# Kernel tuning notes

Hardware: AMD Instinct MI355X
Metric: run time of the kernel (lower is better)

## Reference

```python
import jax, jax.numpy as jnp
import numpy as np


def setup_inputs() -> dict:
    key = jax.random.key(0)
    k1, k2 = jax.random.split(key)
    T, D, K = 100000, 768, 500  # frames, feature dim (HuBERT base), k-means clusters
    feat = jax.random.normal(k1, (T, D), dtype=jnp.float32)
    C = jax.random.normal(k2, (D, K), dtype=jnp.float32)  # cluster centers, transposed as in module
    return {"feat": feat, "C": C}


def reference(feat, C):
    # Squared euclidean distance expanded: ||f||^2 - 2 f.C + ||c||^2
    Cnorm = jnp.sum(C * C, axis=0, keepdims=True)            # [1, K]
    fnorm = jnp.sum(feat * feat, axis=1, keepdims=True)       # [T, 1]
    dist = fnorm - 2.0 * jnp.matmul(feat, C) + Cnorm          # [T, K]
    return jnp.argmin(dist, axis=1)[None, :]                  # [1, T] cluster ids
```

## Files before the change

### kernel.cpp

```cpp
#include <hip/hip_runtime.h>
#include <float.h>

#define D_DIM 768
#define K_DIM 500
#define NDT   24
#define BM    64
#define NTH   256
#define PB_STRIDE 100352

typedef _Float16 f16x8  __attribute__((ext_vector_type(8)));
typedef float    f32x16 __attribute__((ext_vector_type(16)));


__global__ void cnorm_partial_kernel(const float* __restrict__ C,
                                     double* __restrict__ partial, int K) {
    const int k = threadIdx.x;
    const int w = blockIdx.x;
    double s = 0.0;
    if (k < K) {
        const int d0 = w * (D_DIM / 16);
        for (int d = d0; d < d0 + (D_DIM / 16); ++d) {
            const float c = C[(size_t)d * K + k];
            s = fma((double)c, (double)c, s);
        }
    }
    partial[w * 512 + k] = s;
}

__global__ void cnorm_finish_kernel(const double* __restrict__ partial,
                                    float* __restrict__ cnorm, int K) {
    const int k = threadIdx.x;
    if (k < K) {
        double s = 0.0;
        for (int w = 0; w < 16; ++w) s += partial[w * 512 + k];
        cnorm[k] = (float)s;
    } else {
        cnorm[k] = FLT_MAX;
    }
}

__global__ void packB_kernel(const float* __restrict__ C,
                             _Float16* __restrict__ BpH,
                             _Float16* __restrict__ BpL) {
    const int idx = blockIdx.x * 256 + threadIdx.x;
    const int col = idx & 511;
    const int dt  = idx >> 9;
    f16x8 h[4], l[4];
    #pragma unroll
    for (int c = 0; c < 4; ++c)
        #pragma unroll
        for (int j = 0; j < 8; ++j) {
            const int k = c * 8 + j;
            const float v = (col < K_DIM)
                          ? C[(size_t)(dt * 32 + k) * K_DIM + col] : 0.0f;
            const _Float16 hh = (_Float16)v;
            h[c][j] = hh;
            l[c][j] = (_Float16)(v - (float)hh);
        }
    f16x8* dH = (f16x8*)(BpH + ((size_t)dt * 512 + col) * 32);
    f16x8* dL = (f16x8*)(BpL + ((size_t)dt * 512 + col) * 32);
    #pragma unroll
    for (int c = 0; c < 4; ++c) { dH[c] = h[c]; dL[c] = l[c]; }
}

__launch_bounds__(NTH, 3)
__global__ void assign_kernel(const float* __restrict__ feat,
                              const _Float16* __restrict__ BpH,
                              const _Float16* __restrict__ BpL,
                              const float* __restrict__ cnorm,
                              float* __restrict__ pbv,
                              int* __restrict__ pbi,
                              int T) {
    __shared__ __align__(16) _Float16 AsH[2][BM * 32];
    __shared__ __align__(16) _Float16 AsL[2][BM * 32];
    __shared__ float red_v[BM * 4];
    __shared__ int   red_i[BM * 4];

    const int tid  = threadIdx.x;
    const int wn   = tid >> 6;
    const int lane = tid & 63;
    const int c5   = lane & 31;
    const int kh   = lane >> 5;
    const int bid  = blockIdx.x;
    const int half = bid & 1;
    const int R0   = (bid >> 1) * BM;

    const int ar = tid >> 2;
    const int ac = (tid & 3) << 3;
    const bool arow_ok = (R0 + ar) < T;
    const float* fptr = feat + (size_t)(R0 + ar) * D_DIM + ac;
    const int asl = ((ac >> 3) + (ar >> 1)) & 3;

    const int colbase = half * 256 + wn * 64 + c5;
    const _Float16* bpH = BpH + (size_t)colbase * 32 + kh * 8;
    const _Float16* bpL = BpL + (size_t)colbase * 32 + kh * 8;

    f32x16 acc[2][2];
    #pragma unroll
    for (int m = 0; m < 2; ++m)
        #pragma unroll
        for (int n = 0; n < 2; ++n)
            #pragma unroll
            for (int r = 0; r < 16; ++r) acc[m][n][r] = 0.0f;

    {
        float4 v0 = make_float4(0.f, 0.f, 0.f, 0.f), v1 = v0;
        if (arow_ok) {
            v0 = *(const float4*)(fptr);
            v1 = *(const float4*)(fptr + 4);
        }
        const float fa[8] = {v0.x, v0.y, v0.z, v0.w, v1.x, v1.y, v1.z, v1.w};
        f16x8 h, l;
        #pragma unroll
        for (int j = 0; j < 8; ++j) {
            const _Float16 hh = (_Float16)fa[j];
            h[j] = hh; l[j] = (_Float16)(fa[j] - (float)hh);
        }
        ((f16x8*)AsH[0])[ar * 4 + asl] = h;
        ((f16x8*)AsL[0])[ar * 4 + asl] = l;
    }
    __syncthreads();

    for (int dt = 0; dt < NDT; ++dt) {
        const int cur = dt & 1;
        const bool hasNext = (dt + 1) < NDT;

        const size_t bo = (size_t)dt * 16384;
        f16x8 bH[2][2], bL[2][2];
        #pragma unroll
        for (int n = 0; n < 2; ++n)
            #pragma unroll
            for (int step = 0; step < 2; ++step) {
                bH[n][step] = *(const f16x8*)(bpH + bo + n * 1024 + step * 16);
                bL[n][step] = *(const f16x8*)(bpL + bo + n * 1024 + step * 16);
            }

        float4 v0 = make_float4(0.f, 0.f, 0.f, 0.f), v1 = v0;
        if (hasNext && arow_ok) {
            v0 = *(const float4*)(fptr + (dt + 1) * 32);
            v1 = *(const float4*)(fptr + (dt + 1) * 32 + 4);
        }

        f16x8 aH[2][2], aL[2][2];
        #pragma unroll
        for (int m = 0; m < 2; ++m) {
            const int row = m * 32 + c5;
            #pragma unroll
            for (int step = 0; step < 2; ++step) {
                const int chunk = step * 2 + kh;
                const int sl = (chunk + (row >> 1)) & 3;
                aH[m][step] = ((const f16x8*)AsH[cur])[row * 4 + sl];
                aL[m][step] = ((const f16x8*)AsL[cur])[row * 4 + sl];
            }
        }

        __builtin_amdgcn_s_setprio(1);
        #pragma unroll
        for (int step = 0; step < 2; ++step)
            #pragma unroll
            for (int n = 0; n < 2; ++n)
                #pragma unroll
                for (int m = 0; m < 2; ++m) {
                    f32x16 a = acc[m][n];
                    a = __builtin_amdgcn_mfma_f32_32x32x16_f16(aH[m][step], bH[n][step], a, 0, 0, 0);
                    a = __builtin_amdgcn_mfma_f32_32x32x16_f16(aL[m][step], bH[n][step], a, 0, 0, 0);
                    a = __builtin_amdgcn_mfma_f32_32x32x16_f16(aH[m][step], bL[n][step], a, 0, 0, 0);
                    acc[m][n] = a;
                }
        __builtin_amdgcn_s_setprio(0);

        if (hasNext) {
            const float fa[8] = {v0.x, v0.y, v0.z, v0.w, v1.x, v1.y, v1.z, v1.w};
            f16x8 h, l;
            #pragma unroll
            for (int j = 0; j < 8; ++j) {
                const _Float16 hh = (_Float16)fa[j];
                h[j] = hh; l[j] = (_Float16)(fa[j] - (float)hh);
            }
            ((f16x8*)AsH[cur ^ 1])[ar * 4 + asl] = h;
            ((f16x8*)AsL[cur ^ 1])[ar * 4 + asl] = l;
        }
        __syncthreads();
    }

    float cn[2];
    #pragma unroll
    for (int n = 0; n < 2; ++n)
        cn[n] = cnorm[half * 256 + wn * 64 + n * 32 + c5];

    #pragma unroll
    for (int m = 0; m < 2; ++m) {
        #pragma unroll
        for (int r = 0; r < 16; ++r) {
            float best = cn[0] - 2.0f * acc[m][0][r];
            int   bi   = colbase;
            {
                const float s = cn[1] - 2.0f * acc[m][1][r];
                const int col = colbase + 32;
                if (s < best) { best = s; bi = col; }
            }
            #pragma unroll
            for (int msk = 1; msk < 32; msk <<= 1) {
                const float ov = __shfl_xor(best, msk, 64);
                const int   oi = __shfl_xor(bi,   msk, 64);
                if (ov < best || (ov == best && oi < bi)) { best = ov; bi = oi; }
            }
            if (c5 == 0) {
                const int rl = m * 32 + 4 * kh + (r & 3) + 8 * (r >> 2);
                red_v[rl * 4 + wn] = best;
                red_i[rl * 4 + wn] = bi;
            }
        }
    }
    __syncthreads();

    if (tid < BM) {
        float bv = red_v[tid * 4];
        int   bi = red_i[tid * 4];
        #pragma unroll
        for (int w = 1; w < 4; ++w) {
            const float v = red_v[tid * 4 + w];
            const int   i = red_i[tid * 4 + w];
            if (v < bv || (v == bv && i < bi)) { bv = v; bi = i; }
        }
        const int r = R0 + tid;
        if (r < T) {
            pbv[(size_t)half * PB_STRIDE + r] = bv;
            pbi[(size_t)half * PB_STRIDE + r] = bi;
        }
    }
}

__global__ void combine_kernel(const float* __restrict__ pbv,
                               const int* __restrict__ pbi,
                               int* __restrict__ out, int T) {
    const int r = blockIdx.x * 256 + threadIdx.x;
    if (r < T) {
        const float s0 = pbv[r];
        const int   i0 = pbi[r];
        const float s1 = pbv[PB_STRIDE + r];
        const int   i1 = pbi[PB_STRIDE + r];
        out[r] = (s1 < s0) ? i1 : i0;
    }
}

extern "C" void kernel_launch(void* const* d_in, const int* in_sizes, int n_in,
                              void* d_out, int out_size, void* d_ws, size_t ws_size,
                              hipStream_t stream) {
    const float* feat = (const float*)d_in[0];
    const float* C    = (const float*)d_in[1];
    int* out          = (int*)d_out;
    const int T = in_sizes[0] / D_DIM;
    const int K = in_sizes[1] / D_DIM;

    float*     cnorm   = (float*)d_ws;
    double*    partial = (double*)((char*)d_ws + 4096);
    _Float16*  BpH     = (_Float16*)((char*)d_ws + 131072);
    _Float16*  BpL     = (_Float16*)((char*)d_ws + 917504);
    float*     pbv     = (float*)((char*)d_ws + 1703936);
    int*       pbi     = (int*)((char*)d_ws + 2506752);

    hipLaunchKernelGGL(cnorm_partial_kernel, dim3(16), dim3(512), 0, stream,
                       C, partial, K);
    hipLaunchKernelGGL(cnorm_finish_kernel, dim3(1), dim3(512), 0, stream,
                       partial, cnorm, K);
    hipLaunchKernelGGL(packB_kernel, dim3(48), dim3(256), 0, stream,
                       C, BpH, BpL);

    const int nrb = (T + BM - 1) / BM;
    hipLaunchKernelGGL(assign_kernel, dim3(nrb * 2), dim3(NTH), 0, stream,
                       feat, BpH, BpL, cnorm, pbv, pbi, T);
    hipLaunchKernelGGL(combine_kernel, dim3((T + 255) / 256), dim3(256), 0, stream,
                       pbv, pbi, out, T);
}
```

Baseline: 326.3 us.

## Load feature operand directly from global into registers, dropping LDS staging

The A operand is no longer staged through double-buffered shared memory with a per-step barrier. Each lane now reads its own rows of feat straight from global memory and splits them into fp16 hi/lo parts in registers. This removes the LDS traffic and the __syncthreads per K step. In exchange, each of the four waves redundantly loads and converts the same 64 rows, so global/L2 reads of feat rise about fourfold, and loads are no longer prefetched one step ahead.

```diff
diff --git a/kernel.cpp b/kernel.cpp
--- a/kernel.cpp
+++ b/kernel.cpp
@@ -71,8 +71,6 @@
                               float* __restrict__ pbv,
                               int* __restrict__ pbi,
                               int T) {
-    __shared__ __align__(16) _Float16 AsH[2][BM * 32];
-    __shared__ __align__(16) _Float16 AsL[2][BM * 32];
     __shared__ float red_v[BM * 4];
     __shared__ int   red_i[BM * 4];
 
@@ -85,15 +83,14 @@
     const int half = bid & 1;
     const int R0   = (bid >> 1) * BM;
 
-    const int ar = tid >> 2;
-    const int ac = (tid & 3) << 3;
-    const bool arow_ok = (R0 + ar) < T;
-    const float* fptr = feat + (size_t)(R0 + ar) * D_DIM + ac;
-    const int asl = ((ac >> 3) + (ar >> 1)) & 3;
+    int r0 = R0 + c5;      r0 = r0 < T ? r0 : T - 1;
+    int r1 = R0 + 32 + c5; r1 = r1 < T ? r1 : T - 1;
+    const float* apA = feat + (size_t)r0 * D_DIM + kh * 8;
+    const float* apB = feat + (size_t)r1 * D_DIM + kh * 8;
 
     const int colbase = half * 256 + wn * 64 + c5;
-    const _Float16* bpH = BpH + (size_t)colbase * 32 + kh * 8;
-    const _Float16* bpL = BpL + (size_t)colbase * 32 + kh * 8;
+    const _Float16* bph = BpH + (size_t)colbase * 32 + kh * 8;
+    const _Float16* bpl = BpL + (size_t)colbase * 32 + kh * 8;
 
     f32x16 acc[2][2];
     #pragma unroll
@@ -103,85 +100,75 @@
             #pragma unroll
             for (int r = 0; r < 16; ++r) acc[m][n][r] = 0.0f;
 
-    {
-        float4 v0 = make_float4(0.f, 0.f, 0.f, 0.f), v1 = v0;
-        if (arow_ok) {
-            v0 = *(const float4*)(fptr);
-            v1 = *(const float4*)(fptr + 4);
-        }
-        const float fa[8] = {v0.x, v0.y, v0.z, v0.w, v1.x, v1.y, v1.z, v1.w};
-        f16x8 h, l;
-        #pragma unroll
-        for (int j = 0; j < 8; ++j) {
-            const _Float16 hh = (_Float16)fa[j];
-            h[j] = hh; l[j] = (_Float16)(fa[j] - (float)hh);
-        }
-        ((f16x8*)AsH[0])[ar * 4 + asl] = h;
-        ((f16x8*)AsL[0])[ar * 4 + asl] = l;
-    }
-    __syncthreads();
-
+#define SPLIT8(V0, V1, H, L) do {                                              \
+    const float fa_[8] = {(V0).x, (V0).y, (V0).z, (V0).w,                      \
+                          (V1).x, (V1).y, (V1).z, (V1).w};                     \
+    _Pragma("unroll")                                                          \
+    for (int j = 0; j < 8; ++j) {                                              \
+        const _Float16 hh = (_Float16)fa_[j];                                  \
+        (H)[j] = hh; (L)[j] = (_Float16)(fa_[j] - (float)hh);                  \
+    }                                                                          \
+} while (0)
+
+    #pragma unroll 1
     for (int dt = 0; dt < NDT; ++dt) {
-        const int cur = dt & 1;
-        const bool hasNext = (dt + 1) < NDT;
+        const float* pa = apA + dt * 32;
+        const float* pb = apB + dt * 32;
+        const float4 ra0 = *(const float4*)(pa);
+        const float4 ra1 = *(const float4*)(pa + 4);
+        const float4 ra2 = *(const float4*)(pa + 16);
+        const float4 ra3 = *(const float4*)(pa + 20);
+        const float4 rb0 = *(const float4*)(pb);
+        const float4 rb1 = *(const float4*)(pb + 4);
+        const float4 rb2 = *(const float4*)(pb + 16);
+        const float4 rb3 = *(const float4*)(pb + 20);
 
         const size_t bo = (size_t)dt * 16384;
-        f16x8 bH[2][2], bL[2][2];
-        #pragma unroll
-        for (int n = 0; n < 2; ++n)
-            #pragma unroll
-            for (int step = 0; step < 2; ++step) {
-                bH[n][step] = *(const f16x8*)(bpH + bo + n * 1024 + step * 16);
-                bL[n][step] = *(const f16x8*)(bpL + bo + n * 1024 + step * 16);
-            }
-
-        float4 v0 = make_float4(0.f, 0.f, 0.f, 0.f), v1 = v0;
-        if (hasNext && arow_ok) {
-            v0 = *(const float4*)(fptr + (dt + 1) * 32);
-            v1 = *(const float4*)(fptr + (dt + 1) * 32 + 4);
-        }
+        const f16x8 b0H0 = *(const f16x8*)(bph + bo);
+        const f16x8 b0H1 = *(const f16x8*)(bph + bo + 1024);
+        const f16x8 b0L0 = *(const f16x8*)(bpl + bo);
+        const f16x8 b0L1 = *(const f16x8*)(bpl + bo + 1024);
 
         f16x8 aH[2][2], aL[2][2];
-        #pragma unroll
-        for (int m = 0; m < 2; ++m) {
-            const int row = m * 32 + c5;
-            #pragma unroll
-            for (int step = 0; step < 2; ++step) {
-                const int chunk = step * 2 + kh;
-                const int sl = (chunk + (row >> 1)) & 3;
-                aH[m][step] = ((const f16x8*)AsH[cur])[row * 4 + sl];
-                aL[m][step] = ((const f16x8*)AsL[cur])[row * 4 + sl];
-            }
-        }
+        SPLIT8(ra0, ra1, aH[0][0], aL[0][0]);
+        SPLIT8(ra2, ra3, aH[0][1], aL[0][1]);
+        SPLIT8(rb0, rb1, aH[1][0], aL[1][0]);
+        SPLIT8(rb2, rb3, aH[1][1], aL[1][1]);
+
+        const f16x8 b1H0 = *(const f16x8*)(bph + bo + 16);
+        const f16x8 b1H1 = *(const f16x8*)(bph + bo + 1024 + 16);
+        const f16x8 b1L0 = *(const f16x8*)(bpl + bo + 16);
+        const f16x8 b1L1 = *(const f16x8*)(bpl + bo + 1024 + 16);
 
         __builtin_amdgcn_s_setprio(1);
-        #pragma unroll
-        for (int step = 0; step < 2; ++step)
-            #pragma unroll
-            for (int n = 0; n < 2; ++n)
-                #pragma unroll
-                for (int m = 0; m < 2; ++m) {
-                    f32x16 a = acc[m][n];
-                    a = __builtin_amdgcn_mfma_f32_32x32x16_f16(aH[m][step], bH[n][step], a, 0, 0, 0);
-                    a = __builtin_amdgcn_mfma_f32_32x32x16_f16(aL[m][step], bH[n][step], a, 0, 0, 0);
-                    a = __builtin_amdgcn_mfma_f32_32x32x16_f16(aH[m][step], bL[n][step], a, 0, 0, 0);
-                    acc[m][n] = a;
-                }
+        acc[0][0] = __builtin_amdgcn_mfma_f32_32x32x16_f16(aH[0][0], b0H0, acc[0][0], 0, 0, 0);
+        acc[0][0] = __builtin_amdgcn_mfma_f32_32x32x16_f16(aL[0][0], b0H0, acc[0][0], 0, 0, 0);
+        acc[0][0] = __builtin_amdgcn_mfma_f32_32x32x16_f16(aH[0][0], b0L0, acc[0][0], 0, 0, 0);
+        acc[1][0] = __builtin_amdgcn_mfma_f32_32x32x16_f16(aH[1][0], b0H0, acc[1][0], 0, 0, 0);
+        acc[1][0] = __builtin_amdgcn_mfma_f32_32x32x16_f16(aL[1][0], b0H0, acc[1][0], 0, 0, 0);
+        acc[1][0] = __builtin_amdgcn_mfma_f32_32x32x16_f16(aH[1][0], b0L0, acc[1][0], 0, 0, 0);
+        acc[0][1] = __builtin_amdgcn_mfma_f32_32x32x16_f16(aH[0][0], b0H1, acc[0][1], 0, 0, 0);
+        acc[0][1] = __builtin_amdgcn_mfma_f32_32x32x16_f16(aL[0][0], b0H1, acc[0][1], 0, 0, 0);
+        acc[0][1] = __builtin_amdgcn_mfma_f32_32x32x16_f16(aH[0][0], b0L1, acc[0][1], 0, 0, 0);
+        acc[1][1] = __builtin_amdgcn_mfma_f32_32x32x16_f16(aH[1][0], b0H1, acc[1][1], 0, 0, 0);
+        acc[1][1] = __builtin_amdgcn_mfma_f32_32x32x16_f16(aL[1][0], b0H1, acc[1][1], 0, 0, 0);
+        acc[1][1] = __builtin_amdgcn_mfma_f32_32x32x16_f16(aH[1][0], b0L1, acc[1][1], 0, 0, 0);
+
+        acc[0][0] = __builtin_amdgcn_mfma_f32_32x32x16_f16(aH[0][1], b1H0, acc[0][0], 0, 0, 0);
+        acc[0][0] = __builtin_amdgcn_mfma_f32_32x32x16_f16(aL[0][1], b1H0, acc[0][0], 0, 0, 0);
+        acc[0][0] = __builtin_amdgcn_mfma_f32_32x32x16_f16(aH[0][1], b1L0, acc[0][0], 0, 0, 0);
+        acc[1][0] = __builtin_amdgcn_mfma_f32_32x32x16_f16(aH[1][1], b1H0, acc[1][0], 0, 0, 0);
+        acc[1][0] = __builtin_amdgcn_mfma_f32_32x32x16_f16(aL[1][1], b1H0, acc[1][0], 0, 0, 0);
+        acc[1][0] = __builtin_amdgcn_mfma_f32_32x32x16_f16(aH[1][1], b1L0, acc[1][0], 0, 0, 0);
+        acc[0][1] = __builtin_amdgcn_mfma_f32_32x32x16_f16(aH[0][1], b1H1, acc[0][1], 0, 0, 0);
+        acc[0][1] = __builtin_amdgcn_mfma_f32_32x32x16_f16(aL[0][1], b1H1, acc[0][1], 0, 0, 0);
+        acc[0][1] = __builtin_amdgcn_mfma_f32_32x32x16_f16(aH[0][1], b1L1, acc[0][1], 0, 0, 0);
+        acc[1][1] = __builtin_amdgcn_mfma_f32_32x32x16_f16(aH[1][1], b1H1, acc[1][1], 0, 0, 0);
+        acc[1][1] = __builtin_amdgcn_mfma_f32_32x32x16_f16(aL[1][1], b1H1, acc[1][1], 0, 0, 0);
+        acc[1][1] = __builtin_amdgcn_mfma_f32_32x32x16_f16(aH[1][1], b1L1, acc[1][1], 0, 0, 0);
         __builtin_amdgcn_s_setprio(0);
-
-        if (hasNext) {
-            const float fa[8] = {v0.x, v0.y, v0.z, v0.w, v1.x, v1.y, v1.z, v1.w};
-            f16x8 h, l;
-            #pragma unroll
-            for (int j = 0; j < 8; ++j) {
-                const _Float16 hh = (_Float16)fa[j];
-                h[j] = hh; l[j] = (_Float16)(fa[j] - (float)hh);
-            }
-            ((f16x8*)AsH[cur ^ 1])[ar * 4 + asl] = h;
-            ((f16x8*)AsL[cur ^ 1])[ar * 4 + asl] = l;
-        }
-        __syncthreads();
-    }
+    }
+#undef SPLIT8
 
     float cn[2];
     #pragma unroll
@@ -196,8 +183,7 @@
             int   bi   = colbase;
             {
                 const float s = cn[1] - 2.0f * acc[m][1][r];
-                const int col = colbase + 32;
-                if (s < best) { best = s; bi = col; }
+                if (s < best) { best = s; bi = colbase + 32; }
             }
             #pragma unroll
             for (int msk = 1; msk < 32; msk <<= 1) {
```

Result: slower. 506.5 us (+55.2%).
